# Performance work log

Measured on AMD Instinct MI355X. Metric: run time of the kernel, lower is better.

Reference implementation:

```python
import jax, jax.numpy as jnp
import numpy as np

NUM_POINTS = 72
GAMMA = 2.0
RADIUS = 15.0
W_CLS = 1.0
W_SIM = 3.0
LW_CLS = 2.0
LW_XYTL = 0.5
LW_LIOU = 2.0
K_MAX = 64
EPS = 1e-12  # F.normalize eps


def _normalize(v):
    # F.normalize over the flattened prior axis: v / max(||v||_2, eps)
    return v / jnp.maximum(jnp.linalg.norm(v), EPS)


def _liou_loss(pred, tgt):
    # pred: [..., P], tgt broadcastable; line IoU with radius, loss = 1 - iou
    lo = jnp.minimum(pred, tgt)
    hi = jnp.maximum(pred, tgt)
    ovr = (lo + RADIUS) - (hi - RADIUS)          # per-point overlap (may be < 0)
    union = (hi + RADIUS) - (lo - RADIUS)
    iou = jnp.sum(ovr, -1) / (jnp.sum(union, -1) + 1e-9)
    return 1.0 - iou


def _per_lane(feature, prior):
    # feature: [N, D] predictions for one image; prior: [D] one GT lane
    # ---- assignment cost ----
    logits = feature[:, :2]
    log_s = jax.nn.log_softmax(logits, axis=0)   # softmax over the N priors dim (dim=1 of [1,N,2])
    s = jnp.exp(log_s)
    focal_cost = jnp.sum(((1.0 - s) ** GAMMA) * log_s * prior[:2], axis=-1)  # [N]
    xy_cost = _normalize(jnp.sqrt(jnp.sum((feature[:, 3:5] - prior[3:5]) ** 2, -1)))  # [N]
    theta_cost = _normalize(feature[:, 5] - prior[5])                                  # [N]
    dis_cost = _normalize(jnp.sum(jnp.abs(feature[:, 6:] - prior[6:]), -1) / NUM_POINTS)  # [N]
    cost = W_SIM * (dis_cost * xy_cost * theta_cost) ** 2 + W_CLS * focal_cost
    # ---- dynamic top-k ----
    liou_all = _liou_loss(feature[:, 6:], prior[None, 6:])  # [N]
    k = jnp.clip(jnp.sum(liou_all).astype(jnp.int32), 1, K_MAX)
    _, idx = jax.lax.top_k(-cost, K_MAX)  # sorted ascending by cost; first k == topk(-cost, k)
    mask = (jnp.arange(K_MAX) < k).astype(feature.dtype)  # [K]
    kf = jnp.sum(mask)
    pf = feature[idx]  # [K, D] gathered predicted features
    # ---- xytl smooth-L1 on column-normalized concat([pred[:,2:6]; label[2:6]]) over valid rows ----
    rows = pf[:, 2:6]          # [K, 4]
    lab = prior[2:6]           # [4]
    colnorm = jnp.sqrt(jnp.sum((rows ** 2) * mask[:, None], 0) + lab ** 2)  # norm over the k+1 rows
    denom = jnp.maximum(colnorm, EPS)
    d = rows / denom - lab / denom  # [K, 4]
    ad = jnp.abs(d)
    sl1 = jnp.mean(jnp.where(ad < 1.0, 0.5 * d * d, ad - 0.5), -1)  # [K]
    sl1l = jnp.sum(sl1 * mask) / kf
    # ---- focal cls loss per assigned prior vs argmax of label cls ----
    tgt = jnp.argmax(prior[:2])
    lp = jax.nn.log_softmax(pf[:, :2], axis=-1)  # [K, 2]
    logpt = lp[:, tgt]
    pt = jnp.exp(logpt)
    fl_i = -((1.0 - pt) ** GAMMA) * logpt  # [K]
    fl = jnp.sum(fl_i * mask) / kf
    # ---- LIoU loss on assigned priors ----
    ll_i = _liou_loss(pf[:, 6:], prior[None, 6:])  # [K]
    ll = jnp.sum(ll_i * mask) / kf
    return sl1l, ll, fl


def setup_inputs() -> dict:
    key = jax.random.key(0)
    k1, k2 = jax.random.split(key)
    output = jax.random.normal(k1, (64, 1000, 78), dtype=jnp.float32)
    label = jax.random.normal(k2, (64, 16, 78), dtype=jnp.float32)
    return {"output": output, "label": label}


def reference(output, label):
    per_img = jax.vmap(_per_lane, in_axes=(None, 0))        # over lanes
    sl1l, ll, fl = jax.vmap(per_img, in_axes=(0, 0))(output, label)  # over batch
    sl1l = jnp.mean(sl1l)
    ll = jnp.mean(ll)
    fl = jnp.mean(fl)
    loss = (jnp.where(sl1l > 0, LW_XYTL * sl1l, 0.0)
            + jnp.where(ll > 0, LW_LIOU * ll, 0.0)
            + jnp.where(fl > 0, LW_CLS * fl, 0.0))
    return loss
```

## Files before the change

kernel.cpp:

```cpp
#include <hip/hip_runtime.h>
#include <math.h>

#define NROWS 1000
#define TWO_R_N 2160.0f
typedef unsigned int uint;
typedef unsigned long long ull;

__device__ __forceinline__ float wsumf(float v){
#pragma unroll
  for(int o=32;o;o>>=1) v += __shfl_xor(v,o,64);
  return v;
}
__device__ __forceinline__ float wmaxf(float v){
#pragma unroll
  for(int o=32;o;o>>=1) v = fmaxf(v,__shfl_xor(v,o,64));
  return v;
}

__global__ __launch_bounds__(256,2) void clr_task(const float* __restrict__ feat,
                                                  const float* __restrict__ lab,
                                                  float* __restrict__ ws)
{
  const int b  = blockIdx.x & 63;
  const int pg = blockIdx.x >> 6;
  const float* __restrict__ F  = feat + (size_t)b*NROWS*78;
  const float* __restrict__ PA = lab + ((size_t)b*16 + pg*2)*78;
  const float* __restrict__ PB = PA + 78;

  __shared__ float sS [2][NROWS];
  __shared__ float sRT[2][NROWS];
  __shared__ float sC0[NROWS], sC1[NROWS];
  __shared__ float red[4][8];
  __shared__ int   selIdx[2][64];

  const int tid=threadIdx.x, wave=tid>>6, lane=tid&63;
  const int rloc16=lane>>2, q=lane&3;

  float pva[18], pvb[18];
#pragma unroll
  for(int s=0;s<18;++s){ pva[s]=PA[6+q+4*s]; pvb[s]=PB[6+q+4*s]; }
  const float2* PA2=(const float2*)PA;
  const float2* PB2=(const float2*)PB;
  const float2 a01=PA2[0], a23=PA2[1], a45=PA2[2];
  const float2 b01=PB2[0], b23=PB2[1], b45=PB2[2];

  float accR0=0.f,accT0=0.f,accD0=0.f,accL0=0.f;
  float accR1=0.f,accT1=0.f,accD1=0.f,accL1=0.f;

#pragma unroll 2
  for(int pass=0; pass<16; ++pass){
    const int rr = pass*64 + wave*16 + rloc16;
    if(rr < NROWS){
      const float* __restrict__ rp = F + rr*78;
      float part0=0.f, part1=0.f;
#pragma unroll
      for(int s=0;s<9;++s){
        const float x = rp[6+q+4*s];
        const float y = rp[6+q+4*(s+9)];
        part0 += fabsf(x - pva[s]);
        part0 += fabsf(y - pva[s+9]);
        part1 += fabsf(x - pvb[s]);
        part1 += fabsf(y - pvb[s+9]);
      }
      float s1a=part0+__shfl_xor(part0,1,64);
      float S0 = s1a +__shfl_xor(s1a, 2,64);
      float s1b=part1+__shfl_xor(part1,1,64);
      float S1 = s1b +__shfl_xor(s1b, 2,64);
      if(q==0){
        sS[0][rr]=S0; sS[1][rr]=S1;
        float d0=S0*(1.f/72.f); accD0+=d0*d0;
        accL0 += 1.f-(TWO_R_N-S0)/(TWO_R_N+S0+1e-9f);
        float d1=S1*(1.f/72.f); accD1+=d1*d1;
        accL1 += 1.f-(TWO_R_N-S1)/(TWO_R_N+S1+1e-9f);
      } else if(q==1){
        const float2* rp2=(const float2*)rp;
        const float2 c23=rp2[1], c45=rp2[2];
        float dr3=c23.y-a23.y, dr4=c45.x-a45.x, tt=c45.y-a45.y;
        float r2=dr3*dr3+dr4*dr4;
        sRT[0][rr]=sqrtf(r2)*tt; accR0+=r2; accT0+=tt*tt;
        dr3=c23.y-b23.y; dr4=c45.x-b45.x; tt=c45.y-b45.y;
        r2=dr3*dr3+dr4*dr4;
        sRT[1][rr]=sqrtf(r2)*tt; accR1+=r2; accT1+=tt*tt;
      } else if(q==2){
        const float2* rp2=(const float2*)rp;
        const float2 c01=rp2[0];
        sC0[rr]=c01.x; sC1[rr]=c01.y;
      }
    }
  }

  {
    float vR0=wsumf(accR0), vT0=wsumf(accT0), vD0=wsumf(accD0), vL0=wsumf(accL0);
    float vR1=wsumf(accR1), vT1=wsumf(accT1), vD1=wsumf(accD1), vL1=wsumf(accL1);
    if(lane==0){
      red[wave][0]=vR0; red[wave][1]=vT0; red[wave][2]=vD0; red[wave][3]=vL0;
      red[wave][4]=vR1; red[wave][5]=vT1; red[wave][6]=vD1; red[wave][7]=vL1;
    }
  }
  __syncthreads();
  if(wave>=2) return;
  const int w = wave;

  float R=0.f,T=0.f,D=0.f,L=0.f;
#pragma unroll
  for(int g=0;g<4;++g){
    R+=red[g][4*w]; T+=red[g][4*w+1]; D+=red[g][4*w+2]; L+=red[g][4*w+3];
  }
  float Nr=fmaxf(sqrtf(R),1e-12f), Nt=fmaxf(sqrtf(T),1e-12f), Nd=fmaxf(sqrtf(D),1e-12f);
  const float inv = 1.f/(Nr*Nt*Nd);
  int k=(int)L; if(k<1)k=1; if(k>64)k=64;

  float m0=-INFINITY, m1=-INFINITY;
#pragma unroll
  for(int t=0;t<16;++t){ int i=t*64+lane; if(i<NROWS){ m0=fmaxf(m0,sC0[i]); m1=fmaxf(m1,sC1[i]); } }
  m0=wmaxf(m0); m1=wmaxf(m1);
  float s0=0.f, s1=0.f;
#pragma unroll
  for(int t=0;t<16;++t){ int i=t*64+lane; if(i<NROWS){ s0+=__expf(sC0[i]-m0); s1+=__expf(sC1[i]-m1); } }
  s0=wsumf(s0); s1=wsumf(s1);
  const float lse0=m0+__logf(s0), lse1=m1+__logf(s1);

  const float2 p01 = w ? b01 : a01;
  const float2 p23 = w ? b23 : a23;
  const float2 p45 = w ? b45 : a45;

  uint key[16];
  const float p0=p01.x, pp1=p01.y;
#pragma unroll
  for(int t=0;t<16;++t){
    int i=t*64+lane; uint kk=0xFFFFFFFFu;
    if(i<NROWS){
      float ls0=sC0[i]-lse0, ls1=sC1[i]-lse1;
      float e0=__expf(ls0), e1=__expf(ls1);
      float focal=(1.f-e0)*(1.f-e0)*ls0*p0 + (1.f-e1)*(1.f-e1)*ls1*pp1;
      float prod=sRT[w][i]*(sS[w][i]*(1.f/72.f))*inv;
      float cost=3.f*prod*prod+focal;
      uint x=__float_as_uint(cost);
      kk=(x&0x80000000u)?~x:(x|0x80000000u);
    }
    key[t]=kk;
  }

  uint pref=0u, r=(uint)k;
  for(int s=31;s>=0;--s){
    const uint pp=pref>>s;
    uint cnt=0u;
#pragma unroll
    for(int t=0;t<16;++t) cnt += (uint)__popcll(__ballot((key[t]>>s)==pp));
    if(r>cnt){ r-=cnt; pref|=(1u<<s); }
  }
  const uint T2=pref; uint need=r;

  const ull lmask=(1ull<<lane)-1ull;
  int base=0;
#pragma unroll
  for(int t=0;t<16;++t){
    bool lt = key[t]<T2;
    bool eq = key[t]==T2;
    ull meq=__ballot(eq);
    bool eqs = eq && ((uint)__popcll(meq&lmask)<need);
    uint teq=(uint)__popcll(meq);
    need -= (teq<need?teq:need);
    bool ssel = lt||eqs;
    ull ms=__ballot(ssel);
    if(ssel) selIdx[w][base+(int)__popcll(ms&lmask)] = t*64+lane;
    base += (int)__popcll(ms);
  }

  {
    bool act = lane<k;
    int idx = selIdx[w][act?lane:0];
    const float2* R2=(const float2*)(F+(size_t)idx*78);
    float2 g01=R2[0], g23=R2[1], g45=R2[2];
    float S = sS[w][idx];
    float mk = act?1.f:0.f;
    float n2=wsumf(g23.x*g23.x*mk), n3=wsumf(g23.y*g23.y*mk);
    float n4=wsumf(g45.x*g45.x*mk), n5=wsumf(g45.y*g45.y*mk);
    float l2=p23.x, l3=p23.y, l4=p45.x, l5=p45.y;
    float de2=fmaxf(sqrtf(n2+l2*l2),1e-12f);
    float de3=fmaxf(sqrtf(n3+l3*l3),1e-12f);
    float de4=fmaxf(sqrtf(n4+l4*l4),1e-12f);
    float de5=fmaxf(sqrtf(n5+l5*l5),1e-12f);
    float d2=g23.x/de2-l2/de2, d3=g23.y/de3-l3/de3, d4=g45.x/de4-l4/de4, d5=g45.y/de5-l5/de5;
    auto h=[](float d){ float ad=fabsf(d); return ad<1.f ? 0.5f*d*d : ad-0.5f; };
    float sl1 = 0.25f*(h(d2)+h(d3)+h(d4)+h(d5));
    float mm=fmaxf(g01.x,g01.y);
    float lsee=mm+__logf(__expf(g01.x-mm)+__expf(g01.y-mm));
    float logpt=((pp1>p0)?g01.y:g01.x)-lsee;
    float pt=__expf(logpt);
    float fl=-(1.f-pt)*(1.f-pt)*logpt;
    float ll=1.f-(TWO_R_N-S)/(TWO_R_N+S+1e-9f);
    float ssl=wsumf(sl1*mk), sll=wsumf(ll*mk), sfl=wsumf(fl*mk);
    if(lane==0){
      float invk=1.f/(float)k;
      float* o = ws + (size_t)(b*16 + pg*2 + w)*3;
      o[0]=ssl*invk; o[1]=sll*invk; o[2]=sfl*invk;
    }
  }
}

__global__ __launch_bounds__(256) void clr_finalize(const float* __restrict__ ws,
                                                    float* __restrict__ out)
{
  float a=0.f, bsum=0.f, c=0.f;
  for(int i=threadIdx.x;i<1024;i+=256){
    a    += ws[i*3+0];
    bsum += ws[i*3+1];
    c    += ws[i*3+2];
  }
  a=wsumf(a); bsum=wsumf(bsum); c=wsumf(c);
  __shared__ float r[12];
  int wave=threadIdx.x>>6, lane=threadIdx.x&63;
  if(lane==0){ r[wave*3]=a; r[wave*3+1]=bsum; r[wave*3+2]=c; }
  __syncthreads();
  if(threadIdx.x==0){
    float sa=0,sb=0,sc=0;
    for(int w2=0;w2<4;w2++){sa+=r[w2*3];sb+=r[w2*3+1];sc+=r[w2*3+2];}
    float sl1l=sa*(1.f/1024.f), ll=sb*(1.f/1024.f), fl=sc*(1.f/1024.f);
    float loss = (sl1l>0.f ? 0.5f*sl1l : 0.f)
               + (ll  >0.f ? 2.0f*ll   : 0.f)
               + (fl  >0.f ? 2.0f*fl   : 0.f);
    out[0]=loss;
  }
}

extern "C" void kernel_launch(void* const* d_in, const int* in_sizes, int n_in,
                              void* d_out, int out_size, void* d_ws, size_t ws_size,
                              hipStream_t stream)
{
  const float* feat = (const float*)d_in[0];
  const float* lab  = (const float*)d_in[1];
  float* ws  = (float*)d_ws;
  float* out = (float*)d_out;
  hipLaunchKernelGGL(clr_task, dim3(512), dim3(256), 0, stream, feat, lab, ws);
  hipLaunchKernelGGL(clr_finalize, dim3(1), dim3(256), 0, stream, ws, out);
}
```

Baseline: 97.80 us.

## Split per-lane tail into separate 1024-block kernel via global workspace

After: 104.2 us. +6.5%, slower.

```diff
diff --git a/kernel.cpp b/kernel.cpp
--- a/kernel.cpp
+++ b/kernel.cpp
@@ -6,6 +6,11 @@
 typedef unsigned int uint;
 typedef unsigned long long ull;
 
+#define OFF_RTS  1024000
+#define OFF_INV  3072000
+#define OFF_KK   3073024
+#define OFF_OUT3 3074048
+
 __device__ __forceinline__ float wsumf(float v){
 #pragma unroll
   for(int o=32;o;o>>=1) v += __shfl_xor(v,o,64);
@@ -17,21 +22,20 @@
   return v;
 }
 
-__global__ __launch_bounds__(256,2) void clr_task(const float* __restrict__ feat,
-                                                  const float* __restrict__ lab,
-                                                  float* __restrict__ ws)
+__global__ __launch_bounds__(256,2) void clr_phase_a(const float* __restrict__ feat,
+                                                     const float* __restrict__ lab,
+                                                     float* __restrict__ ws)
 {
   const int b  = blockIdx.x & 63;
   const int pg = blockIdx.x >> 6;
   const float* __restrict__ F  = feat + (size_t)b*NROWS*78;
   const float* __restrict__ PA = lab + ((size_t)b*16 + pg*2)*78;
   const float* __restrict__ PB = PA + 78;
-
-  __shared__ float sS [2][NROWS];
-  __shared__ float sRT[2][NROWS];
-  __shared__ float sC0[NROWS], sC1[NROWS];
+  float2* __restrict__ C01  = (float2*)ws + (size_t)(b*8+pg)*NROWS;
+  float2* __restrict__ RTS0 = (float2*)(ws + OFF_RTS) + (size_t)(b*16+pg*2)*NROWS;
+  float2* __restrict__ RTS1 = RTS0 + NROWS;
+
   __shared__ float red[4][8];
-  __shared__ int   selIdx[2][64];
 
   const int tid=threadIdx.x, wave=tid>>6, lane=tid&63;
   const int rloc16=lane>>2, q=lane&3;
@@ -41,8 +45,8 @@
   for(int s=0;s<18;++s){ pva[s]=PA[6+q+4*s]; pvb[s]=PB[6+q+4*s]; }
   const float2* PA2=(const float2*)PA;
   const float2* PB2=(const float2*)PB;
-  const float2 a01=PA2[0], a23=PA2[1], a45=PA2[2];
-  const float2 b01=PB2[0], b23=PB2[1], b45=PB2[2];
+  const float2 a23=PA2[1], a45=PA2[2];
+  const float2 b23=PB2[1], b45=PB2[2];
 
   float accR0=0.f,accT0=0.f,accD0=0.f,accL0=0.f;
   float accR1=0.f,accT1=0.f,accD1=0.f,accL1=0.f;
@@ -67,7 +71,6 @@
       float s1b=part1+__shfl_xor(part1,1,64);
       float S1 = s1b +__shfl_xor(s1b, 2,64);
       if(q==0){
-        sS[0][rr]=S0; sS[1][rr]=S1;
         float d0=S0*(1.f/72.f); accD0+=d0*d0;
         accL0 += 1.f-(TWO_R_N-S0)/(TWO_R_N+S0+1e-9f);
         float d1=S1*(1.f/72.f); accD1+=d1*d1;
@@ -77,14 +80,13 @@
         const float2 c23=rp2[1], c45=rp2[2];
         float dr3=c23.y-a23.y, dr4=c45.x-a45.x, tt=c45.y-a45.y;
         float r2=dr3*dr3+dr4*dr4;
-        sRT[0][rr]=sqrtf(r2)*tt; accR0+=r2; accT0+=tt*tt;
+        RTS0[rr]=make_float2(sqrtf(r2)*tt, S0); accR0+=r2; accT0+=tt*tt;
         dr3=c23.y-b23.y; dr4=c45.x-b45.x; tt=c45.y-b45.y;
         r2=dr3*dr3+dr4*dr4;
-        sRT[1][rr]=sqrtf(r2)*tt; accR1+=r2; accT1+=tt*tt;
+        RTS1[rr]=make_float2(sqrtf(r2)*tt, S1); accR1+=r2; accT1+=tt*tt;
       } else if(q==2){
         const float2* rp2=(const float2*)rp;
-        const float2 c01=rp2[0];
-        sC0[rr]=c01.x; sC1[rr]=c01.y;
+        C01[rr]=rp2[0];
       }
     }
   }
@@ -100,7 +102,6 @@
   __syncthreads();
   if(wave>=2) return;
   const int w = wave;
-
   float R=0.f,T=0.f,D=0.f,L=0.f;
 #pragma unroll
   for(int g=0;g<4;++g){
@@ -109,31 +110,61 @@
   float Nr=fmaxf(sqrtf(R),1e-12f), Nt=fmaxf(sqrtf(T),1e-12f), Nd=fmaxf(sqrtf(D),1e-12f);
   const float inv = 1.f/(Nr*Nt*Nd);
   int k=(int)L; if(k<1)k=1; if(k>64)k=64;
+  if(lane==0){
+    const int prior = b*16 + pg*2 + w;
+    ws[OFF_INV + prior] = inv;
+    ((int*)ws)[OFF_KK + prior] = k;
+  }
+}
+
+__global__ __launch_bounds__(64,1) void clr_tail(const float* __restrict__ feat,
+                                                 const float* __restrict__ lab,
+                                                 float* __restrict__ ws)
+{
+  const int prior = blockIdx.x;
+  const int b  = prior >> 4;
+  const int pw = prior & 15;
+  const int pair = b*8 + (pw>>1);
+  const int lane = threadIdx.x;
+  const float* __restrict__ F = feat + (size_t)b*NROWS*78;
+  const float* __restrict__ P = lab + ((size_t)b*16 + pw)*78;
+  const float2* __restrict__ C01 = (const float2*)ws + (size_t)pair*NROWS;
+  const float2* __restrict__ RTS = (const float2*)(ws + OFF_RTS) + (size_t)prior*NROWS;
+  const float inv = ws[OFF_INV + prior];
+  const int   k   = ((const int*)ws)[OFF_KK + prior];
+
+  __shared__ int selIdx[64];
+
+  float2 c[16], rs[16];
+#pragma unroll
+  for(int t=0;t<16;++t){
+    int i=t*64+lane; int ic = (i<NROWS)? i : (NROWS-1);
+    c[t]=C01[ic]; rs[t]=RTS[ic];
+  }
+
+  const float2* P2=(const float2*)P;
+  const float2 p01=P2[0], p23=P2[1], p45=P2[2];
+  const float p0=p01.x, pp1=p01.y;
 
   float m0=-INFINITY, m1=-INFINITY;
 #pragma unroll
-  for(int t=0;t<16;++t){ int i=t*64+lane; if(i<NROWS){ m0=fmaxf(m0,sC0[i]); m1=fmaxf(m1,sC1[i]); } }
+  for(int t=0;t<16;++t){ int i=t*64+lane; if(i<NROWS){ m0=fmaxf(m0,c[t].x); m1=fmaxf(m1,c[t].y); } }
   m0=wmaxf(m0); m1=wmaxf(m1);
   float s0=0.f, s1=0.f;
 #pragma unroll
-  for(int t=0;t<16;++t){ int i=t*64+lane; if(i<NROWS){ s0+=__expf(sC0[i]-m0); s1+=__expf(sC1[i]-m1); } }
+  for(int t=0;t<16;++t){ int i=t*64+lane; if(i<NROWS){ s0+=__expf(c[t].x-m0); s1+=__expf(c[t].y-m1); } }
   s0=wsumf(s0); s1=wsumf(s1);
   const float lse0=m0+__logf(s0), lse1=m1+__logf(s1);
 
-  const float2 p01 = w ? b01 : a01;
-  const float2 p23 = w ? b23 : a23;
-  const float2 p45 = w ? b45 : a45;
-
   uint key[16];
-  const float p0=p01.x, pp1=p01.y;
 #pragma unroll
   for(int t=0;t<16;++t){
     int i=t*64+lane; uint kk=0xFFFFFFFFu;
     if(i<NROWS){
-      float ls0=sC0[i]-lse0, ls1=sC1[i]-lse1;
+      float ls0=c[t].x-lse0, ls1=c[t].y-lse1;
       float e0=__expf(ls0), e1=__expf(ls1);
       float focal=(1.f-e0)*(1.f-e0)*ls0*p0 + (1.f-e1)*(1.f-e1)*ls1*pp1;
-      float prod=sRT[w][i]*(sS[w][i]*(1.f/72.f))*inv;
+      float prod=rs[t].x*(rs[t].y*(1.f/72.f))*inv;
       float cost=3.f*prod*prod+focal;
       uint x=__float_as_uint(cost);
       kk=(x&0x80000000u)?~x:(x|0x80000000u);
@@ -141,13 +172,22 @@
     key[t]=kk;
   }
 
+  uint xx[16];
+#pragma unroll
+  for(int t=0;t<16;++t) xx[t]=key[t];
   uint pref=0u, r=(uint)k;
+#pragma unroll
   for(int s=31;s>=0;--s){
-    const uint pp=pref>>s;
+    const uint bit=1u<<s;
     uint cnt=0u;
 #pragma unroll
-    for(int t=0;t<16;++t) cnt += (uint)__popcll(__ballot((key[t]>>s)==pp));
-    if(r>cnt){ r-=cnt; pref|=(1u<<s); }
+    for(int t=0;t<16;++t) cnt += (uint)__popcll(__ballot(xx[t]<bit));
+    if(r>cnt){
+      r-=cnt;
+#pragma unroll
+      for(int t=0;t<16;++t) xx[t]^=bit;
+      pref|=bit;
+    }
   }
   const uint T2=pref; uint need=r;
 
@@ -163,16 +203,16 @@
     need -= (teq<need?teq:need);
     bool ssel = lt||eqs;
     ull ms=__ballot(ssel);
-    if(ssel) selIdx[w][base+(int)__popcll(ms&lmask)] = t*64+lane;
+    if(ssel) selIdx[base+(int)__popcll(ms&lmask)] = t*64+lane;
     base += (int)__popcll(ms);
   }
 
   {
     bool act = lane<k;
-    int idx = selIdx[w][act?lane:0];
+    int idx = selIdx[act?lane:0];
     const float2* R2=(const float2*)(F+(size_t)idx*78);
     float2 g01=R2[0], g23=R2[1], g45=R2[2];
-    float S = sS[w][idx];
+    float S = RTS[idx].y;
     float mk = act?1.f:0.f;
     float n2=wsumf(g23.x*g23.x*mk), n3=wsumf(g23.y*g23.y*mk);
     float n4=wsumf(g45.x*g45.x*mk), n5=wsumf(g45.y*g45.y*mk);
@@ -193,7 +233,7 @@
     float ssl=wsumf(sl1*mk), sll=wsumf(ll*mk), sfl=wsumf(fl*mk);
     if(lane==0){
       float invk=1.f/(float)k;
-      float* o = ws + (size_t)(b*16 + pg*2 + w)*3;
+      float* o = ws + OFF_OUT3 + (size_t)prior*3;
       o[0]=ssl*invk; o[1]=sll*invk; o[2]=sfl*invk;
     }
   }
@@ -202,11 +242,12 @@
 __global__ __launch_bounds__(256) void clr_finalize(const float* __restrict__ ws,
                                                     float* __restrict__ out)
 {
+  const float* __restrict__ src = ws + OFF_OUT3;
   float a=0.f, bsum=0.f, c=0.f;
   for(int i=threadIdx.x;i<1024;i+=256){
-    a    += ws[i*3+0];
-    bsum += ws[i*3+1];
-    c    += ws[i*3+2];
+    a    += src[i*3+0];
+    bsum += src[i*3+1];
+    c    += src[i*3+2];
   }
   a=wsumf(a); bsum=wsumf(bsum); c=wsumf(c);
   __shared__ float r[12];
@@ -232,6 +273,7 @@
   const float* lab  = (const float*)d_in[1];
   float* ws  = (float*)d_ws;
   float* out = (float*)d_out;
-  hipLaunchKernelGGL(clr_task, dim3(512), dim3(256), 0, stream, feat, lab, ws);
-  hipLaunchKernelGGL(clr_finalize, dim3(1), dim3(256), 0, stream, ws, out);
-}
+  hipLaunchKernelGGL(clr_phase_a, dim3(512),  dim3(256), 0, stream, feat, lab, ws);
+  hipLaunchKernelGGL(clr_tail,    dim3(1024), dim3(64),  0, stream, feat, lab, ws);
+  hipLaunchKernelGGL(clr_finalize,dim3(1),    dim3(256), 0, stream, ws, out);
+}
```

## Stage row points through LDS with vectorized loads and streamline radix select

Applied to the files above, without the earlier changes.

New measurement: 98.80 us. Within noise of the previous version (+1.0%).

```diff
diff --git a/kernel.cpp b/kernel.cpp
--- a/kernel.cpp
+++ b/kernel.cpp
@@ -3,6 +3,7 @@
 
 #define NROWS 1000
 #define TWO_R_N 2160.0f
+#define XSTRIDE 83
 typedef unsigned int uint;
 typedef unsigned long long ull;
 
@@ -27,6 +28,7 @@
   const float* __restrict__ PA = lab + ((size_t)b*16 + pg*2)*78;
   const float* __restrict__ PB = PA + 78;
 
+  __shared__ float sX[4][16*XSTRIDE];
   __shared__ float sS [2][NROWS];
   __shared__ float sRT[2][NROWS];
   __shared__ float sC0[NROWS], sC1[NROWS];
@@ -35,6 +37,7 @@
 
   const int tid=threadIdx.x, wave=tid>>6, lane=tid&63;
   const int rloc16=lane>>2, q=lane&3;
+  float* __restrict__ xp = &sX[wave][rloc16*XSTRIDE];
 
   float pva[18], pvb[18];
 #pragma unroll
@@ -51,12 +54,22 @@
   for(int pass=0; pass<16; ++pass){
     const int rr = pass*64 + wave*16 + rloc16;
     if(rr < NROWS){
-      const float* __restrict__ rp = F + rr*78;
+      const float* __restrict__ rp = F + (size_t)rr*78;
+      const float2 A0=*(const float2*)(rp+ 6+4*q), B0=*(const float2*)(rp+ 8+4*q);
+      const float2 A1=*(const float2*)(rp+22+4*q), B1=*(const float2*)(rp+24+4*q);
+      const float2 A2=*(const float2*)(rp+38+4*q), B2=*(const float2*)(rp+40+4*q);
+      const float2 A3=*(const float2*)(rp+54+4*q), B3=*(const float2*)(rp+56+4*q);
+      const float2 E =*(const float2*)(rp+70+2*q);
+      xp[ 6+4*q]=A0.x; xp[ 7+4*q]=A0.y; xp[ 8+4*q]=B0.x; xp[ 9+4*q]=B0.y;
+      xp[22+4*q]=A1.x; xp[23+4*q]=A1.y; xp[24+4*q]=B1.x; xp[25+4*q]=B1.y;
+      xp[38+4*q]=A2.x; xp[39+4*q]=A2.y; xp[40+4*q]=B2.x; xp[41+4*q]=B2.y;
+      xp[54+4*q]=A3.x; xp[55+4*q]=A3.y; xp[56+4*q]=B3.x; xp[57+4*q]=B3.y;
+      xp[70+2*q]=E.x;  xp[71+2*q]=E.y;
       float part0=0.f, part1=0.f;
 #pragma unroll
       for(int s=0;s<9;++s){
-        const float x = rp[6+q+4*s];
-        const float y = rp[6+q+4*(s+9)];
+        const float x = xp[ 6+q+4*s];
+        const float y = xp[42+q+4*s];
         part0 += fabsf(x - pva[s]);
         part0 += fabsf(y - pva[s+9]);
         part1 += fabsf(x - pvb[s]);
@@ -110,30 +123,37 @@
   const float inv = 1.f/(Nr*Nt*Nd);
   int k=(int)L; if(k<1)k=1; if(k>64)k=64;
 
+  float cx[16], cy[16], rt_[16], ssv[16];
+#pragma unroll
+  for(int t=0;t<16;++t){
+    int i=t*64+lane; int ic=(i<NROWS)?i:(NROWS-1);
+    cx[t]=sC0[ic]; cy[t]=sC1[ic]; rt_[t]=sRT[w][ic]; ssv[t]=sS[w][ic];
+  }
+
   float m0=-INFINITY, m1=-INFINITY;
 #pragma unroll
-  for(int t=0;t<16;++t){ int i=t*64+lane; if(i<NROWS){ m0=fmaxf(m0,sC0[i]); m1=fmaxf(m1,sC1[i]); } }
+  for(int t=0;t<16;++t){ int i=t*64+lane; if(i<NROWS){ m0=fmaxf(m0,cx[t]); m1=fmaxf(m1,cy[t]); } }
   m0=wmaxf(m0); m1=wmaxf(m1);
   float s0=0.f, s1=0.f;
 #pragma unroll
-  for(int t=0;t<16;++t){ int i=t*64+lane; if(i<NROWS){ s0+=__expf(sC0[i]-m0); s1+=__expf(sC1[i]-m1); } }
+  for(int t=0;t<16;++t){ int i=t*64+lane; if(i<NROWS){ s0+=__expf(cx[t]-m0); s1+=__expf(cy[t]-m1); } }
   s0=wsumf(s0); s1=wsumf(s1);
   const float lse0=m0+__logf(s0), lse1=m1+__logf(s1);
 
   const float2 p01 = w ? b01 : a01;
   const float2 p23 = w ? b23 : a23;
   const float2 p45 = w ? b45 : a45;
+  const float p0=p01.x, pp1=p01.y;
 
   uint key[16];
-  const float p0=p01.x, pp1=p01.y;
 #pragma unroll
   for(int t=0;t<16;++t){
     int i=t*64+lane; uint kk=0xFFFFFFFFu;
     if(i<NROWS){
-      float ls0=sC0[i]-lse0, ls1=sC1[i]-lse1;
+      float ls0=cx[t]-lse0, ls1=cy[t]-lse1;
       float e0=__expf(ls0), e1=__expf(ls1);
       float focal=(1.f-e0)*(1.f-e0)*ls0*p0 + (1.f-e1)*(1.f-e1)*ls1*pp1;
-      float prod=sRT[w][i]*(sS[w][i]*(1.f/72.f))*inv;
+      float prod=rt_[t]*(ssv[t]*(1.f/72.f))*inv;
       float cost=3.f*prod*prod+focal;
       uint x=__float_as_uint(cost);
       kk=(x&0x80000000u)?~x:(x|0x80000000u);
@@ -141,13 +161,22 @@
     key[t]=kk;
   }
 
+  uint xx[16];
+#pragma unroll
+  for(int t=0;t<16;++t) xx[t]=key[t];
   uint pref=0u, r=(uint)k;
+#pragma unroll
   for(int s=31;s>=0;--s){
-    const uint pp=pref>>s;
+    const uint bit=1u<<s;
     uint cnt=0u;
 #pragma unroll
-    for(int t=0;t<16;++t) cnt += (uint)__popcll(__ballot((key[t]>>s)==pp));
-    if(r>cnt){ r-=cnt; pref|=(1u<<s); }
+    for(int t=0;t<16;++t) cnt += (uint)__popcll(__ballot(xx[t]<bit));
+    if(r>cnt){
+      r-=cnt;
+#pragma unroll
+      for(int t=0;t<16;++t) xx[t]^=bit;
+      pref|=bit;
+    }
   }
   const uint T2=pref; uint need=r;
 
```

## Rebalance tail work across waves and stage gathered rows in shared memory

Applied to the files above, without the earlier changes.

Result: slower. 105.4 us (+7.8%).

```diff
diff --git a/kernel.cpp b/kernel.cpp
--- a/kernel.cpp
+++ b/kernel.cpp
@@ -15,6 +15,10 @@
 #pragma unroll
   for(int o=32;o;o>>=1) v = fmaxf(v,__shfl_xor(v,o,64));
   return v;
+}
+__device__ __forceinline__ void wsumf2(float& a, float& b){
+#pragma unroll
+  for(int o=32;o;o>>=1){ float ta=__shfl_xor(a,o,64), tb=__shfl_xor(b,o,64); a+=ta; b+=tb; }
 }
 
 __global__ __launch_bounds__(256,2) void clr_task(const float* __restrict__ feat,
@@ -30,7 +34,9 @@
   __shared__ float sS [2][NROWS];
   __shared__ float sRT[2][NROWS];
   __shared__ float sC0[NROWS], sC1[NROWS];
+  __shared__ float sG[NROWS][4];
   __shared__ float red[4][8];
+  __shared__ float sLse[2];
   __shared__ int   selIdx[2][64];
 
   const int tid=threadIdx.x, wave=tid>>6, lane=tid&63;
@@ -51,7 +57,7 @@
   for(int pass=0; pass<16; ++pass){
     const int rr = pass*64 + wave*16 + rloc16;
     if(rr < NROWS){
-      const float* __restrict__ rp = F + rr*78;
+      const float* __restrict__ rp = F + (size_t)rr*78;
       float part0=0.f, part1=0.f;
 #pragma unroll
       for(int s=0;s<9;++s){
@@ -85,6 +91,10 @@
         const float2* rp2=(const float2*)rp;
         const float2 c01=rp2[0];
         sC0[rr]=c01.x; sC1[rr]=c01.y;
+      } else {
+        const float2* rp2=(const float2*)rp;
+        const float2 c23=rp2[1], c45=rp2[2];
+        sG[rr][0]=c23.x; sG[rr][1]=c23.y; sG[rr][2]=c45.x; sG[rr][3]=c45.y;
       }
     }
   }
@@ -98,103 +108,164 @@
     }
   }
   __syncthreads();
-  if(wave>=2) return;
-  const int w = wave;
-
-  float R=0.f,T=0.f,D=0.f,L=0.f;
-#pragma unroll
-  for(int g=0;g<4;++g){
-    R+=red[g][4*w]; T+=red[g][4*w+1]; D+=red[g][4*w+2]; L+=red[g][4*w+3];
-  }
-  float Nr=fmaxf(sqrtf(R),1e-12f), Nt=fmaxf(sqrtf(T),1e-12f), Nd=fmaxf(sqrtf(D),1e-12f);
-  const float inv = 1.f/(Nr*Nt*Nd);
-  int k=(int)L; if(k<1)k=1; if(k>64)k=64;
-
-  float m0=-INFINITY, m1=-INFINITY;
-#pragma unroll
-  for(int t=0;t<16;++t){ int i=t*64+lane; if(i<NROWS){ m0=fmaxf(m0,sC0[i]); m1=fmaxf(m1,sC1[i]); } }
-  m0=wmaxf(m0); m1=wmaxf(m1);
-  float s0=0.f, s1=0.f;
-#pragma unroll
-  for(int t=0;t<16;++t){ int i=t*64+lane; if(i<NROWS){ s0+=__expf(sC0[i]-m0); s1+=__expf(sC1[i]-m1); } }
-  s0=wsumf(s0); s1=wsumf(s1);
-  const float lse0=m0+__logf(s0), lse1=m1+__logf(s1);
-
-  const float2 p01 = w ? b01 : a01;
-  const float2 p23 = w ? b23 : a23;
-  const float2 p45 = w ? b45 : a45;
-
-  uint key[16];
-  const float p0=p01.x, pp1=p01.y;
+
+  float R0=0.f,T0=0.f,D0=0.f,L0=0.f, R1=0.f,T1=0.f,D1=0.f,L1=0.f;
+  if(wave>=2){
+    const float* __restrict__ col = (wave==2)? sC0 : sC1;
+    float m=-INFINITY;
+#pragma unroll
+    for(int t=0;t<16;++t){ int i=t*64+lane; if(i<NROWS) m=fmaxf(m,col[i]); }
+    m=wmaxf(m);
+    float ssum=0.f;
+#pragma unroll
+    for(int t=0;t<16;++t){ int i=t*64+lane; if(i<NROWS) ssum+=__expf(col[i]-m); }
+    ssum=wsumf(ssum);
+    if(lane==0) sLse[wave-2]=m+__logf(ssum);
+  } else if(wave==0){
+#pragma unroll
+    for(int g=0;g<4;++g){
+      R0+=red[g][0]; T0+=red[g][1]; D0+=red[g][2]; L0+=red[g][3];
+      R1+=red[g][4]; T1+=red[g][5]; D1+=red[g][6]; L1+=red[g][7];
+    }
+  }
+  __syncthreads();
+  if(wave!=0) return;
+
+  float Nr0=fmaxf(sqrtf(R0),1e-12f), Nt0=fmaxf(sqrtf(T0),1e-12f), Nd0=fmaxf(sqrtf(D0),1e-12f);
+  float Nr1=fmaxf(sqrtf(R1),1e-12f), Nt1=fmaxf(sqrtf(T1),1e-12f), Nd1=fmaxf(sqrtf(D1),1e-12f);
+  const float inv0=1.f/(Nr0*Nt0*Nd0), inv1=1.f/(Nr1*Nt1*Nd1);
+  int k0=(int)L0; if(k0<1)k0=1; if(k0>64)k0=64;
+  int k1=(int)L1; if(k1<1)k1=1; if(k1>64)k1=64;
+  const float lse0=sLse[0], lse1=sLse[1];
+  const float pa0=a01.x, pa1=a01.y;
+  const float pb0=b01.x, pb1=b01.y;
+
+  uint key0[16], key1[16];
 #pragma unroll
   for(int t=0;t<16;++t){
-    int i=t*64+lane; uint kk=0xFFFFFFFFu;
+    int i=t*64+lane; uint kA=0xFFFFFFFFu, kB=0xFFFFFFFFu;
     if(i<NROWS){
       float ls0=sC0[i]-lse0, ls1=sC1[i]-lse1;
       float e0=__expf(ls0), e1=__expf(ls1);
-      float focal=(1.f-e0)*(1.f-e0)*ls0*p0 + (1.f-e1)*(1.f-e1)*ls1*pp1;
-      float prod=sRT[w][i]*(sS[w][i]*(1.f/72.f))*inv;
-      float cost=3.f*prod*prod+focal;
-      uint x=__float_as_uint(cost);
-      kk=(x&0x80000000u)?~x:(x|0x80000000u);
-    }
-    key[t]=kk;
-  }
-
-  uint pref=0u, r=(uint)k;
+      float w0=(1.f-e0)*(1.f-e0)*ls0, w1=(1.f-e1)*(1.f-e1)*ls1;
+      float rt0=sRT[0][i], ss0=sS[0][i], rt1=sRT[1][i], ss1=sS[1][i];
+      float focalA=w0*pa0+w1*pa1;
+      float prodA=rt0*(ss0*(1.f/72.f))*inv0;
+      float costA=3.f*prodA*prodA+focalA;
+      uint xA=__float_as_uint(costA);
+      kA=(xA&0x80000000u)?~xA:(xA|0x80000000u);
+      float focalB=w0*pb0+w1*pb1;
+      float prodB=rt1*(ss1*(1.f/72.f))*inv1;
+      float costB=3.f*prodB*prodB+focalB;
+      uint xB=__float_as_uint(costB);
+      kB=(xB&0x80000000u)?~xB:(xB|0x80000000u);
+    }
+    key0[t]=kA; key1[t]=kB;
+  }
+
+  uint xx0[16], xx1[16];
+#pragma unroll
+  for(int t=0;t<16;++t){ xx0[t]=key0[t]; xx1[t]=key1[t]; }
+  uint pref0=0u, r0=(uint)k0, pref1=0u, r1=(uint)k1;
+#pragma unroll
   for(int s=31;s>=0;--s){
-    const uint pp=pref>>s;
-    uint cnt=0u;
-#pragma unroll
-    for(int t=0;t<16;++t) cnt += (uint)__popcll(__ballot((key[t]>>s)==pp));
-    if(r>cnt){ r-=cnt; pref|=(1u<<s); }
-  }
-  const uint T2=pref; uint need=r;
+    const uint bit=1u<<s;
+    uint c0=0u, c1=0u;
+#pragma unroll
+    for(int t=0;t<16;++t){
+      c0 += (uint)__popcll(__ballot(xx0[t]<bit));
+      c1 += (uint)__popcll(__ballot(xx1[t]<bit));
+    }
+    const uint x0=(r0>c0)?bit:0u, x1=(r1>c1)?bit:0u;
+    r0 -= (r0>c0)?c0:0u;  r1 -= (r1>c1)?c1:0u;
+    pref0|=x0; pref1|=x1;
+#pragma unroll
+    for(int t=0;t<16;++t){ xx0[t]^=x0; xx1[t]^=x1; }
+  }
+  const uint TA=pref0, TB=pref1;
+  uint need0=r0, need1=r1;
 
   const ull lmask=(1ull<<lane)-1ull;
-  int base=0;
+  int base0=0, base1=0;
 #pragma unroll
   for(int t=0;t<16;++t){
-    bool lt = key[t]<T2;
-    bool eq = key[t]==T2;
-    ull meq=__ballot(eq);
-    bool eqs = eq && ((uint)__popcll(meq&lmask)<need);
-    uint teq=(uint)__popcll(meq);
-    need -= (teq<need?teq:need);
-    bool ssel = lt||eqs;
-    ull ms=__ballot(ssel);
-    if(ssel) selIdx[w][base+(int)__popcll(ms&lmask)] = t*64+lane;
-    base += (int)__popcll(ms);
+    {
+      bool lt = key0[t]<TA;
+      bool eq = key0[t]==TA;
+      ull meq=__ballot(eq);
+      bool eqs = eq && ((uint)__popcll(meq&lmask)<need0);
+      uint teq=(uint)__popcll(meq);
+      need0 -= (teq<need0?teq:need0);
+      bool ssel = lt||eqs;
+      ull ms=__ballot(ssel);
+      if(ssel) selIdx[0][base0+(int)__popcll(ms&lmask)] = t*64+lane;
+      base0 += (int)__popcll(ms);
+    }
+    {
+      bool lt = key1[t]<TB;
+      bool eq = key1[t]==TB;
+      ull meq=__ballot(eq);
+      bool eqs = eq && ((uint)__popcll(meq&lmask)<need1);
+      uint teq=(uint)__popcll(meq);
+      need1 -= (teq<need1?teq:need1);
+      bool ssel = lt||eqs;
+      ull ms=__ballot(ssel);
+      if(ssel) selIdx[1][base1+(int)__popcll(ms&lmask)] = t*64+lane;
+      base1 += (int)__popcll(ms);
+    }
   }
 
   {
-    bool act = lane<k;
-    int idx = selIdx[w][act?lane:0];
-    const float2* R2=(const float2*)(F+(size_t)idx*78);
-    float2 g01=R2[0], g23=R2[1], g45=R2[2];
-    float S = sS[w][idx];
-    float mk = act?1.f:0.f;
-    float n2=wsumf(g23.x*g23.x*mk), n3=wsumf(g23.y*g23.y*mk);
-    float n4=wsumf(g45.x*g45.x*mk), n5=wsumf(g45.y*g45.y*mk);
-    float l2=p23.x, l3=p23.y, l4=p45.x, l5=p45.y;
-    float de2=fmaxf(sqrtf(n2+l2*l2),1e-12f);
-    float de3=fmaxf(sqrtf(n3+l3*l3),1e-12f);
-    float de4=fmaxf(sqrtf(n4+l4*l4),1e-12f);
-    float de5=fmaxf(sqrtf(n5+l5*l5),1e-12f);
-    float d2=g23.x/de2-l2/de2, d3=g23.y/de3-l3/de3, d4=g45.x/de4-l4/de4, d5=g45.y/de5-l5/de5;
+    bool act0=lane<k0, act1=lane<k1;
+    int idx0=selIdx[0][act0?lane:0], idx1=selIdx[1][act1?lane:0];
+    float2 g01_0=make_float2(sC0[idx0], sC1[idx0]);
+    float2 g23_0=make_float2(sG[idx0][0], sG[idx0][1]);
+    float2 g45_0=make_float2(sG[idx0][2], sG[idx0][3]);
+    float  S_0  = sS[0][idx0];
+    float2 g01_1=make_float2(sC0[idx1], sC1[idx1]);
+    float2 g23_1=make_float2(sG[idx1][0], sG[idx1][1]);
+    float2 g45_1=make_float2(sG[idx1][2], sG[idx1][3]);
+    float  S_1  = sS[1][idx1];
+    float mk0=act0?1.f:0.f, mk1=act1?1.f:0.f;
+    float n2_0=g23_0.x*g23_0.x*mk0, n2_1=g23_1.x*g23_1.x*mk1; wsumf2(n2_0,n2_1);
+    float n3_0=g23_0.y*g23_0.y*mk0, n3_1=g23_1.y*g23_1.y*mk1; wsumf2(n3_0,n3_1);
+    float n4_0=g45_0.x*g45_0.x*mk0, n4_1=g45_1.x*g45_1.x*mk1; wsumf2(n4_0,n4_1);
+    float n5_0=g45_0.y*g45_0.y*mk0, n5_1=g45_1.y*g45_1.y*mk1; wsumf2(n5_0,n5_1);
     auto h=[](float d){ float ad=fabsf(d); return ad<1.f ? 0.5f*d*d : ad-0.5f; };
-    float sl1 = 0.25f*(h(d2)+h(d3)+h(d4)+h(d5));
-    float mm=fmaxf(g01.x,g01.y);
-    float lsee=mm+__logf(__expf(g01.x-mm)+__expf(g01.y-mm));
-    float logpt=((pp1>p0)?g01.y:g01.x)-lsee;
-    float pt=__expf(logpt);
-    float fl=-(1.f-pt)*(1.f-pt)*logpt;
-    float ll=1.f-(TWO_R_N-S)/(TWO_R_N+S+1e-9f);
-    float ssl=wsumf(sl1*mk), sll=wsumf(ll*mk), sfl=wsumf(fl*mk);
+    float de2=fmaxf(sqrtf(n2_0+a23.x*a23.x),1e-12f);
+    float de3=fmaxf(sqrtf(n3_0+a23.y*a23.y),1e-12f);
+    float de4=fmaxf(sqrtf(n4_0+a45.x*a45.x),1e-12f);
+    float de5=fmaxf(sqrtf(n5_0+a45.y*a45.y),1e-12f);
+    float d2=g23_0.x/de2-a23.x/de2, d3=g23_0.y/de3-a23.y/de3;
+    float d4=g45_0.x/de4-a45.x/de4, d5=g45_0.y/de5-a45.y/de5;
+    float sl1_0 = 0.25f*(h(d2)+h(d3)+h(d4)+h(d5));
+    float mm0=fmaxf(g01_0.x,g01_0.y);
+    float lsee0=mm0+__logf(__expf(g01_0.x-mm0)+__expf(g01_0.y-mm0));
+    float logpt0=((pa1>pa0)?g01_0.y:g01_0.x)-lsee0;
+    float pt0=__expf(logpt0);
+    float fl_0=-(1.f-pt0)*(1.f-pt0)*logpt0;
+    float ll_0=1.f-(TWO_R_N-S_0)/(TWO_R_N+S_0+1e-9f);
+    float e2=fmaxf(sqrtf(n2_1+b23.x*b23.x),1e-12f);
+    float e3=fmaxf(sqrtf(n3_1+b23.y*b23.y),1e-12f);
+    float e4=fmaxf(sqrtf(n4_1+b45.x*b45.x),1e-12f);
+    float e5=fmaxf(sqrtf(n5_1+b45.y*b45.y),1e-12f);
+    float f2=g23_1.x/e2-b23.x/e2, f3=g23_1.y/e3-b23.y/e3;
+    float f4=g45_1.x/e4-b45.x/e4, f5=g45_1.y/e5-b45.y/e5;
+    float sl1_1 = 0.25f*(h(f2)+h(f3)+h(f4)+h(f5));
+    float mm1=fmaxf(g01_1.x,g01_1.y);
+    float lsee1=mm1+__logf(__expf(g01_1.x-mm1)+__expf(g01_1.y-mm1));
+    float logpt1=((pb1>pb0)?g01_1.y:g01_1.x)-lsee1;
+    float pt1=__expf(logpt1);
+    float fl_1=-(1.f-pt1)*(1.f-pt1)*logpt1;
+    float ll_1=1.f-(TWO_R_N-S_1)/(TWO_R_N+S_1+1e-9f);
+    float ssl0=sl1_0*mk0, ssl1=sl1_1*mk1; wsumf2(ssl0,ssl1);
+    float sll0=ll_0 *mk0, sll1=ll_1 *mk1; wsumf2(sll0,sll1);
+    float sfl0=fl_0 *mk0, sfl1=fl_1 *mk1; wsumf2(sfl0,sfl1);
     if(lane==0){
-      float invk=1.f/(float)k;
-      float* o = ws + (size_t)(b*16 + pg*2 + w)*3;
-      o[0]=ssl*invk; o[1]=sll*invk; o[2]=sfl*invk;
+      float* o = ws + (size_t)(b*16 + pg*2)*3;
+      float ik0=1.f/(float)k0, ik1=1.f/(float)k1;
+      o[0]=ssl0*ik0; o[1]=sll0*ik0; o[2]=sfl0*ik0;
+      o[3]=ssl1*ik1; o[4]=sll1*ik1; o[5]=sfl1*ik1;
     }
   }
 }
```
